# Optimization experiments

Measured on AMD Instinct MI355X. Metric: run time of the kernel, lower is better.

The kernel has to match this reference:

```python
import jax, jax.numpy as jnp
import numpy as np
import itertools

NBX = NBY = 6
NUM_BLOCKS = NBX * NBY

def _build_adj():
    adj = []
    for i, j in itertools.product(range(NBX), range(NBY)):
        for dx, dy in [(-1, 0), (0, -1), (0, 1), (1, 0)]:
            x, y = i + dx, j + dy
            if 0 <= x < NBX and 0 <= y < NBY:
                adj.append((j * NBX + i, y * NBX + x))
    return np.array(adj, dtype=np.int32)

ADJ = _build_adj()                                   # [E=120, 2] (src, dst)
NUM_EDGES = ADJ.shape[0]
# composition structure: edge e' can be extended by edge e iff dst(e') == src(e)
COMP = (ADJ[:, 1][:, None] == ADJ[:, 0][None, :]).astype(np.float32)  # [E, E]
MAX_PATH_LEN = NUM_BLOCKS                            # 36 fixed-point iterations


def setup_inputs() -> dict:
    key = jax.random.key(0)
    ks = jax.random.split(key, 10)
    w = lambda k, shape: jax.random.normal(k, shape, jnp.float32) * 0.05
    d = {}
    d["image"] = jax.random.normal(ks[0], (1024, 1, 32, 32), jnp.float32)
    d["conv1_w"] = w(ks[1], (32, 1, 5, 5));   d["conv1_b"] = jnp.zeros((32,), jnp.float32)
    d["conv2_w"] = w(ks[2], (32, 32, 5, 5));  d["conv2_b"] = jnp.zeros((32,), jnp.float32)
    d["conv3_w"] = w(ks[3], (64, 32, 5, 5));  d["conv3_b"] = jnp.zeros((64,), jnp.float32)
    d["conv4_w"] = w(ks[4], (64, 64, 5, 5));  d["conv4_b"] = jnp.zeros((64,), jnp.float32)
    d["ep_w1"] = w(ks[5], (256, 256));        d["ep_b1"] = jnp.zeros((256,), jnp.float32)
    d["ep_w2"] = w(ks[6], (NUM_BLOCKS, 256)); d["ep_b2"] = jnp.zeros((NUM_BLOCKS,), jnp.float32)
    d["conn_w1"] = w(ks[7], (256, 256));      d["conn_b1"] = jnp.zeros((256,), jnp.float32)
    d["conn_w2"] = w(ks[8], (NUM_EDGES, 256)); d["conn_b2"] = jnp.zeros((NUM_EDGES,), jnp.float32)
    return d


def _conv(x, w, b):
    y = jax.lax.conv_general_dilated(x, w, (1, 1), 'VALID',
                                     dimension_numbers=('NCHW', 'OIHW', 'NCHW'))
    return y + b[None, :, None, None]


def _pool2(x):
    return jax.lax.reduce_window(x, -jnp.inf, jax.lax.max,
                                 (1, 1, 2, 2), (1, 1, 2, 2), 'VALID')


def reference(image, conv1_w, conv1_b, conv2_w, conv2_b, conv3_w, conv3_b,
              conv4_w, conv4_b, ep_w1, ep_b1, ep_w2, ep_b2,
              conn_w1, conn_b1, conn_w2, conn_b2):
    # --- CNN feature extractor (NCHW, torch-flatten order) ---
    x = _conv(image, conv1_w, conv1_b)      # [B,32,28,28]
    x = _conv(x, conv2_w, conv2_b)          # [B,32,24,24]
    x = _pool2(x)                           # [B,32,12,12]
    x = _conv(x, conv3_w, conv3_b)          # [B,64,8,8]
    x = _conv(x, conv4_w, conv4_b)          # [B,64,4,4]
    x = _pool2(x)                           # [B,64,2,2]
    emb = x.reshape(x.shape[0], -1)         # [B,256]

    # --- heads ---
    conn = jax.nn.sigmoid(jax.nn.relu(emb @ conn_w1.T + conn_b1) @ conn_w2.T + conn_b2)  # [B,E]
    ep = jax.nn.sigmoid(jax.nn.relu(emb @ ep_w1.T + ep_b1) @ ep_w2.T + ep_b2)            # [B,36]

    # --- recursive path building under DAMP semiring (add=clipped sum, mult=product) ---
    comp = jnp.asarray(COMP)                # [E,E]: dst(e')==src(e)
    def step(carry, _):
        old, recent = carry
        # extend_path/extend_path_cond: new symbol is the edge itself, prob = (sum_paths_ending_at_src) * p_edge
        new = jnp.clip(recent @ comp, 0.0, 1.0) * conn   # [B,E]
        merged = jnp.clip(old + new, 0.0, 1.0)           # merge (|) with DAMP add
        return (merged, new), None
    (merged, _), _ = jax.lax.scan(step, (conn, conn), None, length=MAX_PATH_LEN)

    # is_endpoint: apply_if with first_index_check / last_index_check (semiring mult)
    src = jnp.asarray(ADJ[:, 0])
    dst = jnp.asarray(ADJ[:, 1])
    paths = merged * ep[:, src] * ep[:, dst]             # [B,E]
    return paths[:, 0]
```

## Files before the change

kernel.cpp:

```cpp
#include <hip/hip_runtime.h>
#include <math.h>

typedef __attribute__((ext_vector_type(8))) short short8;
typedef __attribute__((ext_vector_type(4))) float float4v;
typedef __attribute__((ext_vector_type(4))) unsigned short ushort4v;

static __device__ __forceinline__ unsigned short f2bf(float f) {
    union { float f; unsigned u; } v; v.f = f;
    unsigned u = v.u;
    return (unsigned short)((u + 0x7fffu + ((u >> 16) & 1u)) >> 16);
}
static __device__ __forceinline__ float bf2f(unsigned short h) {
    union { unsigned u; float f; } v; v.u = ((unsigned)h) << 16;
    return v.f;
}
static __device__ __forceinline__ unsigned pk2(float a, float b) {
    return (unsigned)f2bf(a) | ((unsigned)f2bf(b) << 16);
}

struct AdjT {
    int src[120];
    int dst[120];
    int cnt[36];
    int idx[36][4];
    int ostart[36];
    int ocnt[36];
};

constexpr AdjT build_adj() {
    AdjT a{};
    const int ddx[4] = {-1, 0, 0, 1};
    const int ddy[4] = {0, -1, 1, 0};
    int ne = 0;
    for (int i = 0; i < 6; i++)
        for (int j = 0; j < 6; j++)
            for (int d = 0; d < 4; d++) {
                int x = i + ddx[d], y = j + ddy[d];
                if (x >= 0 && x < 6 && y >= 0 && y < 6) {
                    a.src[ne] = j * 6 + i;
                    a.dst[ne] = y * 6 + x;
                    ne++;
                }
            }
    for (int n = 0; n < 36; n++) {
        a.cnt[n] = 0;
        for (int e = 0; e < 120; e++)
            if (a.dst[e] == n) a.idx[n][a.cnt[n]++] = e;
    }
    for (int n = 0; n < 36; n++) { a.ostart[n] = 0; a.ocnt[n] = 0; }
    for (int e = 0; e < 120; e++) {
        a.ocnt[a.src[e]]++;
        if (e == 0 || a.src[e] != a.src[e - 1]) a.ostart[a.src[e]] = e;
    }
    return a;
}

__device__ constexpr AdjT ADJC = build_adj();
__device__ constexpr int G16_START[17] =
    {0, 3, 6, 9, 12, 14, 16, 18, 20, 22, 24, 26, 28, 30, 32, 34, 36};

__global__ __launch_bounds__(256) void k_prepall(
    const float* __restrict__ w1, const float* __restrict__ b1,
    const float* __restrict__ w2, const float* __restrict__ b2,
    const float* __restrict__ w3, const float* __restrict__ w4,
    const float* __restrict__ cnw1, const float* __restrict__ epw1,
    const float* __restrict__ cnw2, const float* __restrict__ epw2,
    unsigned short* __restrict__ wpc, float* __restrict__ wcb,
    unsigned short* __restrict__ wp3, unsigned short* __restrict__ wp4,
    unsigned short* __restrict__ wph1, unsigned short* __restrict__ wpcn2,
    unsigned short* __restrict__ wpep2) {
    __shared__ float s_w1[800];
    __shared__ float s_w2[800];
    if (blockIdx.x < 32) {
        const int co = blockIdx.x, tid = threadIdx.x;
        for (int i = tid; i < 800; i += 256) {
            s_w1[i] = w1[i];
            s_w2[i] = w2[co * 800 + i];
        }
        __syncthreads();
        if (tid < 96) {
            int t = tid;
            float val = 0.f;
            if (t < 81) {
                int ty = t / 9, tx = t - 9 * ty;
                int ylo = ty > 4 ? ty - 4 : 0, yhi = ty < 4 ? ty : 4;
                int xlo = tx > 4 ? tx - 4 : 0, xhi = tx < 4 ? tx : 4;
                for (int k1y = ylo; k1y <= yhi; k1y++)
                    for (int k1x = xlo; k1x <= xhi; k1x++) {
                        int o1 = k1y * 5 + k1x;
                        int o2 = (ty - k1y) * 5 + (tx - k1x);
#pragma unroll
                        for (int ci = 0; ci < 32; ci++)
                            val += s_w1[ci * 25 + o1] * s_w2[ci * 25 + o2];
                    }
            }
            int n = co >> 1, nt = co & 1;
            int ks = t >> 5, r = t & 31, q = r >> 3, j = r & 7;
            wpc[ks * 1024 + nt * 512 + (q * 16 + n) * 8 + j] = f2bf(val);
        } else if (tid == 96) {
            float s = b2[co];
            for (int ci = 0; ci < 32; ci++) {
                float ws = 0.f;
#pragma unroll
                for (int t2 = 0; t2 < 25; t2++) ws += s_w2[ci * 25 + t2];
                s += b1[ci] * ws;
            }
            wcb[co] = s;
        }
        return;
    }
    int e = (blockIdx.x - 32) * 256 + threadIdx.x;
    if (e < 51200) {
        int j = e & 7, lane = (e >> 3) & 63, nt = (e >> 9) & 3, t = e >> 11;
        int co = 4 * (lane & 15) + nt, ci = (lane >> 4) * 8 + j;
        wp3[e] = f2bf(w3[(co * 32 + ci) * 25 + t]);
    } else if (e < 153600) {
        int e4 = e - 51200;
        int j = e4 & 7, lane = (e4 >> 3) & 63, nt = (e4 >> 9) & 3;
        int ks = (e4 >> 11) & 1, t = e4 >> 12;
        int co = 4 * (lane & 15) + nt, ci = ks * 32 + (lane >> 4) * 8 + j;
        wp4[e4] = f2bf(w4[(co * 64 + ci) * 25 + t]);
    } else {
        int eh = e - 153600;
        if (eh < 131072) {
            int j = eh & 7, lane = (eh >> 3) & 63, nt = (eh >> 9) & 31, kt = eh >> 14;
            int c = nt * 16 + (lane & 15);
            int k = kt * 32 + ((lane >> 4) << 3) + j;
            float v = (c < 256) ? cnw1[c * 256 + k] : epw1[(c - 256) * 256 + k];
            wph1[eh] = f2bf(v);
        } else if (eh < 163840) {
            int e2 = eh - 131072;
            int j = e2 & 7, lane = (e2 >> 3) & 63, nt = (e2 >> 9) & 7, kt = e2 >> 12;
            int c = nt * 16 + (lane & 15);
            int k = kt * 32 + ((lane >> 4) << 3) + j;
            wpcn2[e2] = f2bf(c < 120 ? cnw2[c * 256 + k] : 0.f);
        } else {
            int e3 = eh - 163840;
            int j = e3 & 7, lane = (e3 >> 3) & 63, idx = e3 >> 9;
            int kt = idx / 3, nt = idx - kt * 3;
            int c = nt * 16 + (lane & 15);
            int k = kt * 32 + ((lane >> 4) << 3) + j;
            wpep2[e3] = f2bf(c < 36 ? epw2[c * 256 + k] : 0.f);
        }
    }
}

#define IMG_REG 10368
#define C3O 5760

__global__ __launch_bounds__(512) void k_convall(
    const float* __restrict__ img,
    const unsigned short* __restrict__ wpc, const float* __restrict__ wcb,
    const unsigned short* __restrict__ wp3, const float* __restrict__ b3,
    const unsigned short* __restrict__ wp4, const float* __restrict__ b4,
    unsigned short* __restrict__ emb) {
    extern __shared__ __align__(16) unsigned short s_dyn[];
    const int b4i = blockIdx.x, tid = threadIdx.x;
    const int lane = tid & 63, wave = tid >> 6;
    const int m = lane & 15, quad = lane >> 4;

#pragma unroll
    for (int ii = 0; ii < 2; ii++) {
        int t4 = tid + ii * 512;
        int simg = t4 >> 8, t = t4 & 255;
        float4 v = ((const float4*)(img + (size_t)(4 * b4i + simg) * 1024))[t];
        ushort4v pkv;
        pkv[0] = f2bf(v.x); pkv[1] = f2bf(v.y);
        pkv[2] = f2bf(v.z); pkv[3] = f2bf(v.w);
        *(ushort4v*)(s_dyn + simg * IMG_REG + C3O + (t >> 3) * 36 + (t & 7) * 4) = pkv;
    }

    const short8* wqc = (const short8*)wpc;
    short8 cb0[3], cb1[3];
#pragma unroll
    for (int ks = 0; ks < 3; ks++) {
        cb0[ks] = wqc[(ks * 2 + 0) * 64 + lane];
        cb1[ks] = wqc[(ks * 2 + 1) * 64 + lane];
    }
    const float bc0 = wcb[2 * m], bc1 = wcb[2 * m + 1];
    int ct[3][8];
#pragma unroll
    for (int ks = 0; ks < 3; ks++)
#pragma unroll
        for (int j = 0; j < 8; j++) {
            int t = ks * 32 + quad * 8 + j;
            int toff = 0;
            if (t < 81) {
                int ty = (t * 57) >> 9;
                toff = ty * 36 + (t - 9 * ty);
            }
            ct[ks][j] = toff;
        }
    const short8* wq3 = (const short8*)wp3;

    __syncthreads();

    for (int TT = wave; TT < 144; TT += 8) {
        int ci = TT / 36;
        int T = TT - 36 * ci;
        int pg = T * 4 + (m >> 2);
        int py = (pg * 171) >> 11;
        int px = pg - py * 12;
        int wb = ci * IMG_REG + C3O + (2 * py + ((m & 3) >> 1)) * 36 + 2 * px + (m & 1);
        float4v a0 = {0.f, 0.f, 0.f, 0.f};
        float4v a1 = {0.f, 0.f, 0.f, 0.f};
#pragma unroll
        for (int ks = 0; ks < 3; ks++) {
            short8 av;
#pragma unroll
            for (int j = 0; j < 8; j++) av[j] = (short)s_dyn[wb + ct[ks][j]];
            a0 = __builtin_amdgcn_mfma_f32_16x16x32_bf16(av, cb0[ks], a0, 0, 0, 0);
            a1 = __builtin_amdgcn_mfma_f32_16x16x32_bf16(av, cb1[ks], a1, 0, 0, 0);
        }
        float mx0 = fmaxf(fmaxf(a0[0], a0[1]), fmaxf(a0[2], a0[3])) + bc0;
        float mx1 = fmaxf(fmaxf(a1[0], a1[1]), fmaxf(a1[2], a1[3])) + bc1;
        int row = T * 4 + quad;
        *(unsigned*)(s_dyn + ci * IMG_REG + row * 40 + 2 * m) = pk2(mx0, mx1);
    }
    __syncthreads();

    {
        const int ip = wave >> 2;
        const int mt0 = ((wave >> 1) & 1) * 2;
        const int nt0 = (wave & 1) * 2;
        const unsigned short* sb0 = s_dyn + (2 * ip + 0) * IMG_REG;
        const unsigned short* sb1 = s_dyn + (2 * ip + 1) * IMG_REG;
        int a3[2];
#pragma unroll
        for (int mi = 0; mi < 2; mi++) {
            int pos3 = (mt0 + mi) * 16 + m;
            int y3 = pos3 >> 3, x3 = pos3 & 7;
            a3[mi] = (y3 * 12 + x3) * 40 + quad * 8;
        }
        float4v acc3[2][2][2];
#pragma unroll
        for (int im = 0; im < 2; im++)
#pragma unroll
            for (int mi = 0; mi < 2; mi++)
#pragma unroll
                for (int ni = 0; ni < 2; ni++)
                    acc3[im][mi][ni] = (float4v){0.f, 0.f, 0.f, 0.f};
        short8 bA0 = wq3[(0 * 4 + nt0) * 64 + lane];
        short8 bA1 = wq3[(0 * 4 + nt0 + 1) * 64 + lane];
        short8 bB0 = wq3[(1 * 4 + nt0) * 64 + lane];
        short8 bB1 = wq3[(1 * 4 + nt0 + 1) * 64 + lane];
        for (int t = 0; t < 25; t++) {
            short8 bC0, bC1;
            if (t < 23) {
                bC0 = wq3[((t + 2) * 4 + nt0) * 64 + lane];
                bC1 = wq3[((t + 2) * 4 + nt0 + 1) * 64 + lane];
            }
            const int ky = t / 5, kx = t - ky * 5;
            const int toff = (ky * 12 + kx) * 40;
            short8 av00 = *(const short8*)(sb0 + a3[0] + toff);
            short8 av01 = *(const short8*)(sb0 + a3[1] + toff);
            short8 av10 = *(const short8*)(sb1 + a3[0] + toff);
            short8 av11 = *(const short8*)(sb1 + a3[1] + toff);
            acc3[0][0][0] = __builtin_amdgcn_mfma_f32_16x16x32_bf16(av00, bA0, acc3[0][0][0], 0, 0, 0);
            acc3[0][0][1] = __builtin_amdgcn_mfma_f32_16x16x32_bf16(av00, bA1, acc3[0][0][1], 0, 0, 0);
            acc3[0][1][0] = __builtin_amdgcn_mfma_f32_16x16x32_bf16(av01, bA0, acc3[0][1][0], 0, 0, 0);
            acc3[0][1][1] = __builtin_amdgcn_mfma_f32_16x16x32_bf16(av01, bA1, acc3[0][1][1], 0, 0, 0);
            acc3[1][0][0] = __builtin_amdgcn_mfma_f32_16x16x32_bf16(av10, bA0, acc3[1][0][0], 0, 0, 0);
            acc3[1][0][1] = __builtin_amdgcn_mfma_f32_16x16x32_bf16(av10, bA1, acc3[1][0][1], 0, 0, 0);
            acc3[1][1][0] = __builtin_amdgcn_mfma_f32_16x16x32_bf16(av11, bA0, acc3[1][1][0], 0, 0, 0);
            acc3[1][1][1] = __builtin_amdgcn_mfma_f32_16x16x32_bf16(av11, bA1, acc3[1][1][1], 0, 0, 0);
            bA0 = bB0; bA1 = bB1;
            if (t < 23) { bB0 = bC0; bB1 = bC1; }
        }
        float bb0 = b3[4 * m + nt0], bb1 = b3[4 * m + nt0 + 1];
#pragma unroll
        for (int im = 0; im < 2; im++)
#pragma unroll
            for (int mi = 0; mi < 2; mi++)
#pragma unroll
                for (int r = 0; r < 4; r++) {
                    int row3 = (mt0 + mi) * 16 + quad * 4 + r;
                    *(unsigned*)(s_dyn + (2 * ip + im) * IMG_REG + C3O + row3 * 72 + 4 * m + nt0) =
                        pk2(acc3[im][mi][0][r] + bb0, acc3[im][mi][1][r] + bb1);
                }
    }
    __syncthreads();

    {
        const int ip = wave >> 2, nt4 = wave & 3;
        int y4 = m >> 2, x4 = m & 3;
        const unsigned short* sb0 = s_dyn + (2 * ip + 0) * IMG_REG;
        const unsigned short* sb1 = s_dyn + (2 * ip + 1) * IMG_REG;
        int a4 = C3O + (y4 * 8 + x4) * 72 + quad * 8;
        float4v acc4[2];
        acc4[0] = (float4v){0.f, 0.f, 0.f, 0.f};
        acc4[1] = (float4v){0.f, 0.f, 0.f, 0.f};
        const short8* wq4 = (const short8*)wp4;
        short8 cA0 = wq4[((0 * 2 + 0) * 4 + nt4) * 64 + lane];
        short8 cA1 = wq4[((0 * 2 + 1) * 4 + nt4) * 64 + lane];
        short8 cB0 = wq4[((1 * 2 + 0) * 4 + nt4) * 64 + lane];
        short8 cB1 = wq4[((1 * 2 + 1) * 4 + nt4) * 64 + lane];
        for (int t = 0; t < 25; t++) {
            short8 cC0, cC1;
            if (t < 23) {
                cC0 = wq4[(((t + 2) * 2 + 0) * 4 + nt4) * 64 + lane];
                cC1 = wq4[(((t + 2) * 2 + 1) * 4 + nt4) * 64 + lane];
            }
            const int ky = t / 5, kx = t - ky * 5;
            const int toff = (ky * 8 + kx) * 72;
            short8 a00 = *(const short8*)(sb0 + a4 + toff);
            short8 a01 = *(const short8*)(sb0 + a4 + toff + 32);
            short8 a10 = *(const short8*)(sb1 + a4 + toff);
            short8 a11 = *(const short8*)(sb1 + a4 + toff + 32);
            acc4[0] = __builtin_amdgcn_mfma_f32_16x16x32_bf16(a00, cA0, acc4[0], 0, 0, 0);
            acc4[0] = __builtin_amdgcn_mfma_f32_16x16x32_bf16(a01, cA1, acc4[0], 0, 0, 0);
            acc4[1] = __builtin_amdgcn_mfma_f32_16x16x32_bf16(a10, cA0, acc4[1], 0, 0, 0);
            acc4[1] = __builtin_amdgcn_mfma_f32_16x16x32_bf16(a11, cA1, acc4[1], 0, 0, 0);
            cA0 = cB0; cA1 = cB1;
            if (t < 23) { cB0 = cC0; cB1 = cC1; }
        }
#pragma unroll
        for (int im = 0; im < 2; im++) {
            float* s_c4 = (float*)(s_dyn + (2 * ip + im) * IMG_REG);
#pragma unroll
            for (int r = 0; r < 4; r++)
                s_c4[(quad * 4 + r) * 68 + 4 * m + nt4] = acc4[im][r];
        }
    }
    __syncthreads();

#pragma unroll
    for (int ii = 0; ii < 2; ii++) {
        int t4 = tid + ii * 512;
        const int simg = t4 >> 8, t = t4 & 255;
        const float* s_c4 = (const float*)(s_dyn + simg * IMG_REG);
        int co = t >> 2, pp = t & 3;
        int ppy = pp >> 1, ppx = pp & 1;
        float v0 = s_c4[((2 * ppy) * 4 + 2 * ppx) * 68 + co];
        float v1 = s_c4[((2 * ppy) * 4 + 2 * ppx + 1) * 68 + co];
        float v2 = s_c4[((2 * ppy + 1) * 4 + 2 * ppx) * 68 + co];
        float v3 = s_c4[((2 * ppy + 1) * 4 + 2 * ppx + 1) * 68 + co];
        emb[(size_t)(4 * b4i + simg) * 256 + t] =
            f2bf(fmaxf(fmaxf(v0, v1), fmaxf(v2, v3)) + b4[co]);
    }
}

__global__ __launch_bounds__(256) void k_heads(
    const unsigned short* __restrict__ emb,
    const unsigned short* __restrict__ wph1,
    const float* __restrict__ cn_b1, const float* __restrict__ ep_b1,
    const unsigned short* __restrict__ wpcn2, const float* __restrict__ cn_b2,
    const unsigned short* __restrict__ wpep2, const float* __restrict__ ep_b2,
    float* __restrict__ out) {
    __shared__ unsigned short s_hid[16 * 520];
    __shared__ float s_conn[120 * 17];
    __shared__ float s_rec0[120 * 17];
    __shared__ float s_rec1[120 * 17];
    __shared__ float s_ep[36 * 17];
    const int tid = threadIdx.x;
    const int lane = tid & 63, wave = tid >> 6;
    const int m = lane & 15, q = lane >> 4;
    const int b0 = blockIdx.x * 16;

    float4v acc[8];
#pragma unroll
    for (int i = 0; i < 8; i++) acc[i] = (float4v){0.f, 0.f, 0.f, 0.f};
    const short8* wp1 = (const short8*)wph1;
    for (int kt = 0; kt < 8; kt++) {
        short8 av = *(const short8*)(emb + (size_t)(b0 + m) * 256 + kt * 32 + q * 8);
#pragma unroll
        for (int ntl = 0; ntl < 8; ntl++) {
            int nt = wave * 8 + ntl;
            short8 bv = wp1[(kt * 32 + nt) * 64 + lane];
            acc[ntl] = __builtin_amdgcn_mfma_f32_16x16x32_bf16(av, bv, acc[ntl], 0, 0, 0);
        }
    }
#pragma unroll
    for (int ntl = 0; ntl < 8; ntl++) {
        int c = (wave * 8 + ntl) * 16 + m;
        float bb = (c < 256) ? cn_b1[c] : ep_b1[c - 256];
#pragma unroll
        for (int r = 0; r < 4; r++)
            s_hid[(q * 4 + r) * 520 + c] = f2bf(fmaxf(acc[ntl][r] + bb, 0.f));
    }
    __syncthreads();

    for (int job = wave; job < 11; job += 4) {
        const bool isconn = job < 8;
        const int koff = isconn ? 0 : 256;
        float4v a2 = (float4v){0.f, 0.f, 0.f, 0.f};
        for (int kt = 0; kt < 8; kt++) {
            short8 av = *(const short8*)(s_hid + m * 520 + koff + kt * 32 + q * 8);
            short8 bv = isconn
                ? ((const short8*)wpcn2)[(kt * 8 + job) * 64 + lane]
                : ((const short8*)wpep2)[(kt * 3 + (job - 8)) * 64 + lane];
            a2 = __builtin_amdgcn_mfma_f32_16x16x32_bf16(av, bv, a2, 0, 0, 0);
        }
        int c = (isconn ? job : (job - 8)) * 16 + m;
        float bb = isconn ? (c < 120 ? cn_b2[c] : 0.f) : (c < 36 ? ep_b2[c] : 0.f);
#pragma unroll
        for (int r = 0; r < 4; r++) {
            float v = 1.f / (1.f + __expf(-(a2[r] + bb)));
            int row = q * 4 + r;
            if (isconn) {
                if (c < 120) { s_conn[c * 17 + row] = v; s_rec0[c * 17 + row] = v; }
            } else {
                if (c < 36) s_ep[c * 17 + row] = v;
            }
        }
    }
    __syncthreads();

    const int row = tid >> 4, g = tid & 15;
    const int ns = G16_START[g];
    const int nodecnt = G16_START[g + 1] - ns;
    int ie[3][4], icnt[3], os[3], oc[3];
    float cr[3][4];
#pragma unroll
    for (int s = 0; s < 3; s++) {
        if (s < nodecnt) {
            int n = ns + s;
            icnt[s] = ADJC.cnt[n];
#pragma unroll
            for (int qx = 0; qx < 4; qx++) ie[s][qx] = ADJC.idx[n][qx];
            os[s] = ADJC.ostart[n];
            oc[s] = ADJC.ocnt[n];
#pragma unroll
            for (int oe = 0; oe < 4; oe++)
                cr[s][oe] = (oe < oc[s]) ? s_conn[(os[s] + oe) * 17 + row] : 0.f;
        } else {
            icnt[s] = 0; oc[s] = 0; os[s] = 0;
#pragma unroll
            for (int qx = 0; qx < 4; qx++) ie[s][qx] = 0;
#pragma unroll
            for (int oe = 0; oe < 4; oe++) cr[s][oe] = 0.f;
        }
    }
    float old0 = (g == 0) ? s_conn[0 * 17 + row] : 0.f;

    for (int it = 0; it < 36; it++) {
        const float* cur = (it & 1) ? s_rec1 : s_rec0;
        float* nxt = (it & 1) ? s_rec0 : s_rec1;
#pragma unroll
        for (int s = 0; s < 3; s++) {
            float sum = 0.f;
#pragma unroll
            for (int qx = 0; qx < 4; qx++)
                sum += (qx < icnt[s]) ? cur[ie[s][qx] * 17 + row] : 0.f;
            sum = fminf(sum, 1.f);
#pragma unroll
            for (int oe = 0; oe < 4; oe++) {
                if (oe < oc[s]) {
                    int e = os[s] + oe;
                    float nv = sum * cr[s][oe];
                    nxt[e * 17 + row] = nv;
                    if (g == 0 && s == 0 && oe == 0)
                        old0 = fminf(old0 + nv, 1.f);
                }
            }
        }
        __asm__ volatile("s_waitcnt lgkmcnt(0)" ::: "memory");
    }

    if (g == 0)
        out[b0 + row] = old0 * s_ep[0 * 17 + row] * s_ep[6 * 17 + row];
}

extern "C" void kernel_launch(void* const* d_in, const int* in_sizes, int n_in,
                              void* d_out, int out_size, void* d_ws, size_t ws_size,
                              hipStream_t stream) {
    const float* image = (const float*)d_in[0];
    const float* c1w = (const float*)d_in[1];
    const float* c1b = (const float*)d_in[2];
    const float* c2w = (const float*)d_in[3];
    const float* c2b = (const float*)d_in[4];
    const float* c3w = (const float*)d_in[5];
    const float* c3b = (const float*)d_in[6];
    const float* c4w = (const float*)d_in[7];
    const float* c4b = (const float*)d_in[8];
    const float* epw1 = (const float*)d_in[9];
    const float* epb1 = (const float*)d_in[10];
    const float* epw2 = (const float*)d_in[11];
    const float* epb2 = (const float*)d_in[12];
    const float* cnw1 = (const float*)d_in[13];
    const float* cnb1 = (const float*)d_in[14];
    const float* cnw2 = (const float*)d_in[15];
    const float* cnb2 = (const float*)d_in[16];

    const int B = in_sizes[0] / (32 * 32);

    unsigned short* ws = (unsigned short*)d_ws;
    unsigned short* embo = ws;
    unsigned short* wp3 = embo + (size_t)B * 256;
    unsigned short* wp4 = wp3 + 51200;
    unsigned short* wph1 = wp4 + 102400;
    unsigned short* wpcn2 = wph1 + 131072;
    unsigned short* wpep2 = wpcn2 + 32768;
    unsigned short* wpc = wpep2 + 12288;
    float* wcb = (float*)(wpc + 3072);

    const int conv_lds = 4 * IMG_REG * (int)sizeof(unsigned short);
    static int attr_done = 0;
    if (!attr_done) {
        hipFuncSetAttribute((const void*)k_convall,
                            hipFuncAttributeMaxDynamicSharedMemorySize, conv_lds);
        attr_done = 1;
    }

    k_prepall<<<1320, 256, 0, stream>>>(c1w, c1b, c2w, c2b, c3w, c4w,
                                        cnw1, epw1, cnw2, epw2,
                                        wpc, wcb, wp3, wp4, wph1, wpcn2, wpep2);
    k_convall<<<B / 4, 512, conv_lds, stream>>>(image, wpc, wcb, wp3, c3b, wp4, c4b, embo);
    k_heads<<<B / 16, 256, 0, stream>>>(embo, wph1, cnb1, epb1,
                                        wpcn2, cnb2, wpep2, epb2, (float*)d_out);
}
```

Measured before the change: 163.0 us.

## Use shifted image copies for vector LDS gathers and halve images per block

New measurement: 167.6 us. 2.8% more time.

```diff
diff --git a/kernel.cpp b/kernel.cpp
--- a/kernel.cpp
+++ b/kernel.cpp
@@ -9,10 +9,6 @@
     union { float f; unsigned u; } v; v.f = f;
     unsigned u = v.u;
     return (unsigned short)((u + 0x7fffu + ((u >> 16) & 1u)) >> 16);
-}
-static __device__ __forceinline__ float bf2f(unsigned short h) {
-    union { unsigned u; float f; } v; v.u = ((unsigned)h) << 16;
-    return v.f;
 }
 static __device__ __forceinline__ unsigned pk2(float a, float b) {
     return (unsigned)f2bf(a) | ((unsigned)f2bf(b) << 16);
@@ -78,11 +74,11 @@
             s_w2[i] = w2[co * 800 + i];
         }
         __syncthreads();
-        if (tid < 96) {
+        if (tid < 160) {
             int t = tid;
+            int ty = t >> 4, tx = t & 15;
             float val = 0.f;
-            if (t < 81) {
-                int ty = t / 9, tx = t - 9 * ty;
+            if (ty < 9 && tx < 9) {
                 int ylo = ty > 4 ? ty - 4 : 0, yhi = ty < 4 ? ty : 4;
                 int xlo = tx > 4 ? tx - 4 : 0, xhi = tx < 4 ? tx : 4;
                 for (int k1y = ylo; k1y <= yhi; k1y++)
@@ -97,7 +93,7 @@
             int n = co >> 1, nt = co & 1;
             int ks = t >> 5, r = t & 31, q = r >> 3, j = r & 7;
             wpc[ks * 1024 + nt * 512 + (q * 16 + n) * 8 + j] = f2bf(val);
-        } else if (tid == 96) {
+        } else if (tid == 160) {
             float s = b2[co];
             for (int ci = 0; ci < 32; ci++) {
                 float ws = 0.f;
@@ -145,7 +141,7 @@
     }
 }
 
-#define IMG_REG 10368
+#define REGSZ 10560
 #define C3O 5760
 
 __global__ __launch_bounds__(512) void k_convall(
@@ -154,81 +150,98 @@
     const unsigned short* __restrict__ wp3, const float* __restrict__ b3,
     const unsigned short* __restrict__ wp4, const float* __restrict__ b4,
     unsigned short* __restrict__ emb) {
-    extern __shared__ __align__(16) unsigned short s_dyn[];
-    const int b4i = blockIdx.x, tid = threadIdx.x;
+    __shared__ __align__(16) unsigned short s_buf[2 * REGSZ];
+    const int b2 = blockIdx.x, tid = threadIdx.x;
     const int lane = tid & 63, wave = tid >> 6;
     const int m = lane & 15, quad = lane >> 4;
 
-#pragma unroll
-    for (int ii = 0; ii < 2; ii++) {
-        int t4 = tid + ii * 512;
-        int simg = t4 >> 8, t = t4 & 255;
-        float4 v = ((const float4*)(img + (size_t)(4 * b4i + simg) * 1024))[t];
-        ushort4v pkv;
-        pkv[0] = f2bf(v.x); pkv[1] = f2bf(v.y);
-        pkv[2] = f2bf(v.z); pkv[3] = f2bf(v.w);
-        *(ushort4v*)(s_dyn + simg * IMG_REG + C3O + (t >> 3) * 36 + (t & 7) * 4) = pkv;
+    {
+        int simg = tid >> 8, t = tid & 255;
+        float4 v = ((const float4*)(img + (size_t)(2 * b2 + simg) * 1024))[t];
+        unsigned short pv[4];
+        pv[0] = f2bf(v.x); pv[1] = f2bf(v.y);
+        pv[2] = f2bf(v.z); pv[3] = f2bf(v.w);
+        int r = t >> 3, x0 = (t & 7) * 4;
+        int p36 = r * 36 + x0;
+        unsigned short* reg = s_buf + simg * REGSZ + C3O;
+#pragma unroll
+        for (int c = 0; c < 4; c++)
+#pragma unroll
+            for (int i = 0; i < 4; i++) {
+                int pos = p36 + i - c;
+                if (pos >= 0) reg[c * 1200 + pos] = pv[i];
+            }
+    }
+    if (tid < 400) {
+        int simg = tid >= 200, zz = tid - 200 * simg;
+        int r, x;
+        if (zz < 128) { r = zz >> 2; x = 32 + (zz & 3); }
+        else { int rr = zz - 128; r = 32 + (rr >= 36 ? 1 : 0); x = rr - (rr >= 36 ? 36 : 0); }
+        int p36 = r * 36 + x;
+        unsigned short* reg = s_buf + simg * REGSZ + C3O;
+#pragma unroll
+        for (int c = 0; c < 4; c++) {
+            int pos = p36 - c;
+            if (pos >= 0 && pos < 1200) reg[c * 1200 + pos] = 0;
+        }
     }
 
     const short8* wqc = (const short8*)wpc;
-    short8 cb0[3], cb1[3];
-#pragma unroll
-    for (int ks = 0; ks < 3; ks++) {
+    short8 cb0[5], cb1[5];
+#pragma unroll
+    for (int ks = 0; ks < 5; ks++) {
         cb0[ks] = wqc[(ks * 2 + 0) * 64 + lane];
         cb1[ks] = wqc[(ks * 2 + 1) * 64 + lane];
     }
     const float bc0 = wcb[2 * m], bc1 = wcb[2 * m + 1];
-    int ct[3][8];
-#pragma unroll
-    for (int ks = 0; ks < 3; ks++)
-#pragma unroll
-        for (int j = 0; j < 8; j++) {
-            int t = ks * 32 + quad * 8 + j;
-            int toff = 0;
-            if (t < 81) {
-                int ty = (t * 57) >> 9;
-                toff = ty * 36 + (t - 9 * ty);
-            }
-            ct[ks][j] = toff;
-        }
+    int ct2[5];
+#pragma unroll
+    for (int ks = 0; ks < 5; ks++) {
+        int t0 = ks * 32 + quad * 8;
+        ct2[ks] = (t0 >> 4) * 36 + (t0 & 15);
+    }
     const short8* wq3 = (const short8*)wp3;
 
     __syncthreads();
 
-    for (int TT = wave; TT < 144; TT += 8) {
-        int ci = TT / 36;
+    for (int TT = wave; TT < 72; TT += 8) {
+        int ci = TT >= 36 ? 1 : 0;
         int T = TT - 36 * ci;
         int pg = T * 4 + (m >> 2);
         int py = (pg * 171) >> 11;
         int px = pg - py * 12;
-        int wb = ci * IMG_REG + C3O + (2 * py + ((m & 3) >> 1)) * 36 + 2 * px + (m & 1);
+        int albase = (2 * py + ((m & 3) >> 1)) * 36 + 2 * px + (m & 1);
+        const unsigned short* reg = s_buf + ci * REGSZ + C3O;
         float4v a0 = {0.f, 0.f, 0.f, 0.f};
         float4v a1 = {0.f, 0.f, 0.f, 0.f};
 #pragma unroll
-        for (int ks = 0; ks < 3; ks++) {
+        for (int ks = 0; ks < 5; ks++) {
+            int a = albase + ct2[ks];
+            int c = a & 3;
+            const unsigned short* cp = reg + c * 1200 + (a - c);
+            ushort4v lo = *(const ushort4v*)cp;
+            ushort4v hi = *(const ushort4v*)(cp + 4);
             short8 av;
-#pragma unroll
-            for (int j = 0; j < 8; j++) av[j] = (short)s_dyn[wb + ct[ks][j]];
+            av[0] = (short)lo[0]; av[1] = (short)lo[1];
+            av[2] = (short)lo[2]; av[3] = (short)lo[3];
+            av[4] = (short)hi[0]; av[5] = (short)hi[1];
+            av[6] = (short)hi[2]; av[7] = (short)hi[3];
             a0 = __builtin_amdgcn_mfma_f32_16x16x32_bf16(av, cb0[ks], a0, 0, 0, 0);
             a1 = __builtin_amdgcn_mfma_f32_16x16x32_bf16(av, cb1[ks], a1, 0, 0, 0);
         }
         float mx0 = fmaxf(fmaxf(a0[0], a0[1]), fmaxf(a0[2], a0[3])) + bc0;
         float mx1 = fmaxf(fmaxf(a1[0], a1[1]), fmaxf(a1[2], a1[3])) + bc1;
         int row = T * 4 + quad;
-        *(unsigned*)(s_dyn + ci * IMG_REG + row * 40 + 2 * m) = pk2(mx0, mx1);
+        *(unsigned*)(s_buf + ci * REGSZ + row * 40 + 2 * m) = pk2(mx0, mx1);
     }
     __syncthreads();
 
-    {
-        const int ip = wave >> 2;
-        const int mt0 = ((wave >> 1) & 1) * 2;
-        const int nt0 = (wave & 1) * 2;
-        const unsigned short* sb0 = s_dyn + (2 * ip + 0) * IMG_REG;
-        const unsigned short* sb1 = s_dyn + (2 * ip + 1) * IMG_REG;
+    if (wave < 4) {
+        const int mp = wave >> 1, np = wave & 1;
         int a3[2];
 #pragma unroll
         for (int mi = 0; mi < 2; mi++) {
-            int pos3 = (mt0 + mi) * 16 + m;
+            int pos3 = (2 * mp + mi) * 16 + m;
             int y3 = pos3 >> 3, x3 = pos3 & 7;
             a3[mi] = (y3 * 12 + x3) * 40 + quad * 8;
         }
@@ -240,22 +253,22 @@
 #pragma unroll
                 for (int ni = 0; ni < 2; ni++)
                     acc3[im][mi][ni] = (float4v){0.f, 0.f, 0.f, 0.f};
-        short8 bA0 = wq3[(0 * 4 + nt0) * 64 + lane];
-        short8 bA1 = wq3[(0 * 4 + nt0 + 1) * 64 + lane];
-        short8 bB0 = wq3[(1 * 4 + nt0) * 64 + lane];
-        short8 bB1 = wq3[(1 * 4 + nt0 + 1) * 64 + lane];
+        short8 bA0 = wq3[(0 * 4 + 2 * np) * 64 + lane];
+        short8 bA1 = wq3[(0 * 4 + 2 * np + 1) * 64 + lane];
+        short8 bB0 = wq3[(1 * 4 + 2 * np) * 64 + lane];
+        short8 bB1 = wq3[(1 * 4 + 2 * np + 1) * 64 + lane];
         for (int t = 0; t < 25; t++) {
             short8 bC0, bC1;
             if (t < 23) {
-                bC0 = wq3[((t + 2) * 4 + nt0) * 64 + lane];
-                bC1 = wq3[((t + 2) * 4 + nt0 + 1) * 64 + lane];
+                bC0 = wq3[((t + 2) * 4 + 2 * np) * 64 + lane];
+                bC1 = wq3[((t + 2) * 4 + 2 * np + 1) * 64 + lane];
             }
             const int ky = t / 5, kx = t - ky * 5;
             const int toff = (ky * 12 + kx) * 40;
-            short8 av00 = *(const short8*)(sb0 + a3[0] + toff);
-            short8 av01 = *(const short8*)(sb0 + a3[1] + toff);
-            short8 av10 = *(const short8*)(sb1 + a3[0] + toff);
-            short8 av11 = *(const short8*)(sb1 + a3[1] + toff);
+            short8 av00 = *(const short8*)(s_buf + a3[0] + toff);
+            short8 av01 = *(const short8*)(s_buf + a3[1] + toff);
+            short8 av10 = *(const short8*)(s_buf + REGSZ + a3[0] + toff);
+            short8 av11 = *(const short8*)(s_buf + REGSZ + a3[1] + toff);
             acc3[0][0][0] = __builtin_amdgcn_mfma_f32_16x16x32_bf16(av00, bA0, acc3[0][0][0], 0, 0, 0);
             acc3[0][0][1] = __builtin_amdgcn_mfma_f32_16x16x32_bf16(av00, bA1, acc3[0][0][1], 0, 0, 0);
             acc3[0][1][0] = __builtin_amdgcn_mfma_f32_16x16x32_bf16(av01, bA0, acc3[0][1][0], 0, 0, 0);
@@ -267,25 +280,23 @@
             bA0 = bB0; bA1 = bB1;
             if (t < 23) { bB0 = bC0; bB1 = bC1; }
         }
-        float bb0 = b3[4 * m + nt0], bb1 = b3[4 * m + nt0 + 1];
+        float bb0 = b3[4 * m + 2 * np], bb1 = b3[4 * m + 2 * np + 1];
 #pragma unroll
         for (int im = 0; im < 2; im++)
 #pragma unroll
             for (int mi = 0; mi < 2; mi++)
 #pragma unroll
                 for (int r = 0; r < 4; r++) {
-                    int row3 = (mt0 + mi) * 16 + quad * 4 + r;
-                    *(unsigned*)(s_dyn + (2 * ip + im) * IMG_REG + C3O + row3 * 72 + 4 * m + nt0) =
+                    int row3 = (2 * mp + mi) * 16 + quad * 4 + r;
+                    *(unsigned*)(s_buf + im * REGSZ + C3O + row3 * 72 + 4 * m + 2 * np) =
                         pk2(acc3[im][mi][0][r] + bb0, acc3[im][mi][1][r] + bb1);
                 }
     }
     __syncthreads();
 
-    {
-        const int ip = wave >> 2, nt4 = wave & 3;
+    if (wave < 4) {
+        const int nt4 = wave;
         int y4 = m >> 2, x4 = m & 3;
-        const unsigned short* sb0 = s_dyn + (2 * ip + 0) * IMG_REG;
-        const unsigned short* sb1 = s_dyn + (2 * ip + 1) * IMG_REG;
         int a4 = C3O + (y4 * 8 + x4) * 72 + quad * 8;
         float4v acc4[2];
         acc4[0] = (float4v){0.f, 0.f, 0.f, 0.f};
@@ -303,10 +314,10 @@
             }
             const int ky = t / 5, kx = t - ky * 5;
             const int toff = (ky * 8 + kx) * 72;
-            short8 a00 = *(const short8*)(sb0 + a4 + toff);
-            short8 a01 = *(const short8*)(sb0 + a4 + toff + 32);
-            short8 a10 = *(const short8*)(sb1 + a4 + toff);
-            short8 a11 = *(const short8*)(sb1 + a4 + toff + 32);
+            short8 a00 = *(const short8*)(s_buf + a4 + toff);
+            short8 a01 = *(const short8*)(s_buf + a4 + toff + 32);
+            short8 a10 = *(const short8*)(s_buf + REGSZ + a4 + toff);
+            short8 a11 = *(const short8*)(s_buf + REGSZ + a4 + toff + 32);
             acc4[0] = __builtin_amdgcn_mfma_f32_16x16x32_bf16(a00, cA0, acc4[0], 0, 0, 0);
             acc4[0] = __builtin_amdgcn_mfma_f32_16x16x32_bf16(a01, cA1, acc4[0], 0, 0, 0);
             acc4[1] = __builtin_amdgcn_mfma_f32_16x16x32_bf16(a10, cA0, acc4[1], 0, 0, 0);
@@ -316,7 +327,7 @@
         }
 #pragma unroll
         for (int im = 0; im < 2; im++) {
-            float* s_c4 = (float*)(s_dyn + (2 * ip + im) * IMG_REG);
+            float* s_c4 = (float*)(s_buf + im * REGSZ);
 #pragma unroll
             for (int r = 0; r < 4; r++)
                 s_c4[(quad * 4 + r) * 68 + 4 * m + nt4] = acc4[im][r];
@@ -324,18 +335,16 @@
     }
     __syncthreads();
 
-#pragma unroll
-    for (int ii = 0; ii < 2; ii++) {
-        int t4 = tid + ii * 512;
-        const int simg = t4 >> 8, t = t4 & 255;
-        const float* s_c4 = (const float*)(s_dyn + simg * IMG_REG);
+    {
+        const int simg = tid >> 8, t = tid & 255;
+        const float* s_c4 = (const float*)(s_buf + simg * REGSZ);
         int co = t >> 2, pp = t & 3;
         int ppy = pp >> 1, ppx = pp & 1;
         float v0 = s_c4[((2 * ppy) * 4 + 2 * ppx) * 68 + co];
         float v1 = s_c4[((2 * ppy) * 4 + 2 * ppx + 1) * 68 + co];
         float v2 = s_c4[((2 * ppy + 1) * 4 + 2 * ppx) * 68 + co];
         float v3 = s_c4[((2 * ppy + 1) * 4 + 2 * ppx + 1) * 68 + co];
-        emb[(size_t)(4 * b4i + simg) * 256 + t] =
+        emb[(size_t)(2 * b2 + simg) * 256 + t] =
             f2bf(fmaxf(fmaxf(v0, v1), fmaxf(v2, v3)) + b4[co]);
     }
 }
@@ -492,20 +501,12 @@
     unsigned short* wpcn2 = wph1 + 131072;
     unsigned short* wpep2 = wpcn2 + 32768;
     unsigned short* wpc = wpep2 + 12288;
-    float* wcb = (float*)(wpc + 3072);
-
-    const int conv_lds = 4 * IMG_REG * (int)sizeof(unsigned short);
-    static int attr_done = 0;
-    if (!attr_done) {
-        hipFuncSetAttribute((const void*)k_convall,
-                            hipFuncAttributeMaxDynamicSharedMemorySize, conv_lds);
-        attr_done = 1;
-    }
+    float* wcb = (float*)(wpc + 5120);
 
     k_prepall<<<1320, 256, 0, stream>>>(c1w, c1b, c2w, c2b, c3w, c4w,
                                         cnw1, epw1, cnw2, epw2,
                                         wpc, wcb, wp3, wp4, wph1, wpcn2, wpep2);
-    k_convall<<<B / 4, 512, conv_lds, stream>>>(image, wpc, wcb, wp3, c3b, wp4, c4b, embo);
+    k_convall<<<B / 2, 512, 0, stream>>>(image, wpc, wcb, wp3, c3b, wp4, c4b, embo);
     k_heads<<<B / 16, 256, 0, stream>>>(embo, wph1, cnb1, epb1,
                                         wpcn2, cnb2, wpep2, epb2, (float*)d_out);
 }
```
